# Kernel optimization log

Measured on AMD Instinct MI355X. Metric: run time of the kernel, lower is better.

## Reference

```python
import jax, jax.numpy as jnp
import numpy as np


def apply_rope(x):
    # x: [b, h, n, d], d even
    b, h, n, d = x.shape
    half = d // 2
    freqs = jnp.arange(0, half, dtype=x.dtype) / half
    theta = 1.0 / 10000 ** freqs                       # [half]
    positions = jnp.arange(n, dtype=x.dtype)
    angles = positions[:, None] * theta[None, :]       # [n, half]
    cos = jnp.cos(angles)[None, None, :, :]
    sin = jnp.sin(angles)[None, None, :, :]
    x1 = x[..., ::2]
    x2 = x[..., 1::2]
    r1 = x1 * cos - x2 * sin
    r2 = x1 * sin + x2 * cos
    # interleave r1, r2 back into even/odd lanes
    return jnp.stack([r1, r2], axis=-1).reshape(b, h, n, d)


def setup_inputs() -> dict:
    key = jax.random.key(0)
    ks = jax.random.split(key, 4)
    B, N, D = 2, 2048, 1024
    x = jax.random.normal(ks[0], (B, N, D), dtype=jnp.float32)
    w_qkv = jax.random.normal(ks[1], (D, 3 * D), dtype=jnp.float32) * (1.0 / np.sqrt(D))
    b_qkv = jnp.zeros((3 * D,), dtype=jnp.float32)
    w_out = jax.random.normal(ks[2], (D, D), dtype=jnp.float32) * (1.0 / np.sqrt(D))
    b_out = jnp.zeros((D,), dtype=jnp.float32)
    return {"x": x, "w_qkv": w_qkv, "b_qkv": b_qkv, "w_out": w_out, "b_out": b_out}


def reference(x, w_qkv, b_qkv, w_out, b_out):
    B, N, D = x.shape
    H = 16
    hd = D // H
    qkv = x @ w_qkv + b_qkv                            # [B, N, 3D]
    q, k, v = jnp.split(qkv, 3, axis=-1)
    # [B, N, D] -> [B, H, N, hd]
    to_heads = lambda t: t.reshape(B, N, H, hd).transpose(0, 2, 1, 3)
    q, k, v = to_heads(q), to_heads(k), to_heads(v)
    # ELU+1 feature map (applied BEFORE RoPE, as in source)
    q = jax.nn.elu(q) + 1
    k = jax.nn.elu(k) + 1
    rot_q = apply_rope(q)
    rot_k = apply_rope(k)
    attn_num = jnp.einsum('bhid,bhjd->bhij', rot_q, rot_k)   # [B,H,N,N]
    attn_denom = jnp.einsum('bhid,bhjd->bhij', q, k)         # [B,H,N,N]
    attn_weights = attn_num / attn_denom
    # dropout deterministic (train=False)
    out = jnp.einsum('bhij,bhjd->bhid', attn_weights, v)     # [B,H,N,hd]
    out = out.transpose(0, 2, 1, 3).reshape(B, N, D)
    return out @ w_out + b_out
```

## Files before the change

### kernel.cpp

```cpp
#include <hip/hip_runtime.h>
#include <hip/hip_bf16.h>

#define B_   2
#define N_   2048
#define D_   1024
#define H_   16
#define HD   64
#define HALF 32
#define M_   (B_*N_)
#define DQKV (3*D_)

typedef __bf16 bf16x8 __attribute__((ext_vector_type(8)));
typedef float  f32x4  __attribute__((ext_vector_type(4)));
typedef float  f32x16 __attribute__((ext_vector_type(16)));

__device__ __forceinline__ bf16x8 ldfrag(const char* tile, int row, int ch) {
    return *(const bf16x8*)(tile + row * 128 + (((ch) ^ (row & 7)) << 4));
}
__device__ __forceinline__ void stfrag16(char* tile, int row, int ch, uint4 v) {
    *(uint4*)(tile + row * 128 + (((ch) ^ (row & 7)) << 4)) = v;
}

__device__ __forceinline__ unsigned pack2(float a, float b) {
    union { __hip_bfloat16 h; unsigned short s; } x, y;
    x.h = __float2bfloat16(a); y.h = __float2bfloat16(b);
    return (unsigned)x.s | ((unsigned)y.s << 16);
}

__global__ __launch_bounds__(256) void k_tables(float* __restrict__ cos_t,
                                                float* __restrict__ sin_t) {
    int i = blockIdx.x * 256 + threadIdx.x;
    if (i >= N_ * HALF) return;
    int n = i / HALF, j = i % HALF;
    float theta = powf(10000.f, -(float)j / (float)HALF);
    float ang = (float)n * theta;
    cos_t[i] = cosf(ang);
    sin_t[i] = sinf(ang);
}

__global__ __launch_bounds__(256) void k_cvt_x(const float* __restrict__ x,
                                               __hip_bfloat16* __restrict__ xb) {
    int i = blockIdx.x * 256 + threadIdx.x;
    float4 v = ((const float4*)x)[i];
    union { ushort4 u; __hip_bfloat16 h[4]; } o;
    o.h[0] = __float2bfloat16(v.x); o.h[1] = __float2bfloat16(v.y);
    o.h[2] = __float2bfloat16(v.z); o.h[3] = __float2bfloat16(v.w);
    ((ushort4*)xb)[i] = o.u;
}

__global__ __launch_bounds__(256) void k_cvt_t(const float* __restrict__ w,
                                               __hip_bfloat16* __restrict__ wt, int ncols) {
    __shared__ float tile[32][33];
    int n0 = blockIdx.x * 32, k0 = blockIdx.y * 32;
    int tx = threadIdx.x & 31, ty = threadIdx.x >> 5;
#pragma unroll
    for (int i = 0; i < 32; i += 8)
        tile[ty + i][tx] = w[(size_t)(k0 + ty + i) * ncols + n0 + tx];
    __syncthreads();
#pragma unroll
    for (int i = 0; i < 32; i += 8)
        wt[(size_t)(n0 + ty + i) * 1024 + k0 + tx] = __float2bfloat16(tile[tx][ty + i]);
}

__global__ __launch_bounds__(256) void k_qkv(
        const __hip_bfloat16* __restrict__ xb, const __hip_bfloat16* __restrict__ wqT,
        const float* __restrict__ bias,
        const float* __restrict__ cos_t, const float* __restrict__ sin_t,
        __hip_bfloat16* __restrict__ qf, __hip_bfloat16* __restrict__ kf,
        __hip_bfloat16* __restrict__ rq, __hip_bfloat16* __restrict__ rk,
        __hip_bfloat16* __restrict__ vt) {
    __shared__ __align__(16) char sA[128 * 128];
    __shared__ __align__(16) char sB[128 * 128];

    const int t    = threadIdx.x;
    const int m0   = blockIdx.y * 128;
    const int n0w  = blockIdx.x * 128;
    const int lane = t & 63;
    const int lrow = lane & 15;
    const int lgrp = lane >> 4;
    const int wid  = t >> 6;
    const int wr   = wid >> 1;
    const int wc   = wid & 1;

    f32x4 acc[4][4] = {};

    for (int kt = 0; kt < D_ / 64; ++kt) {
        const int k0 = kt * 64;
        __syncthreads();
#pragma unroll
        for (int it = 0; it < 4; ++it) {
            int slot = it * 256 + t;
            int r = slot >> 3, c = slot & 7;
            uint4 av = *(const uint4*)(xb  + (size_t)(m0  + r) * D_ + k0 + c * 8);
            uint4 bv = *(const uint4*)(wqT + (size_t)(n0w + r) * D_ + k0 + c * 8);
            stfrag16(sA, r, c, av);
            stfrag16(sB, r, c, bv);
        }
        __syncthreads();

        bf16x8 bfr[4][2];
#pragma unroll
        for (int fn = 0; fn < 4; ++fn) {
            bfr[fn][0] = ldfrag(sB, wc * 64 + fn * 16 + lrow, lgrp);
            bfr[fn][1] = ldfrag(sB, wc * 64 + fn * 16 + lrow, 4 + lgrp);
        }
#pragma unroll
        for (int fm = 0; fm < 4; ++fm) {
            bf16x8 a0 = ldfrag(sA, wr * 64 + fm * 16 + lrow, lgrp);
            bf16x8 a1 = ldfrag(sA, wr * 64 + fm * 16 + lrow, 4 + lgrp);
#pragma unroll
            for (int fn = 0; fn < 4; ++fn) {
                acc[fm][fn] = __builtin_amdgcn_mfma_f32_16x16x32_bf16(a0, bfr[fn][0], acc[fm][fn], 0, 0, 0);
                acc[fm][fn] = __builtin_amdgcn_mfma_f32_16x16x32_bf16(a1, bfr[fn][1], acc[fm][fn], 0, 0, 0);
            }
        }
    }

#pragma unroll
    for (int fn = 0; fn < 4; ++fn) {
        int c   = n0w + wc * 64 + fn * 16 + lrow;
        int sec = c >> 10;
        int cc  = c & 1023;
        int h   = cc >> 6, dd = cc & 63;
        float bia = bias[c];
#pragma unroll
        for (int fm = 0; fm < 4; ++fm) {
            int mb = m0 + wr * 64 + fm * 16 + lgrp * 4;
            int b  = mb >> 11;
            int n  = mb & (N_ - 1);
            if (sec == 2) {
                union { ushort4 u; __hip_bfloat16 hh[4]; } pk;
#pragma unroll
                for (int r = 0; r < 4; ++r)
                    pk.hh[r] = __float2bfloat16(acc[fm][fn][r] + bia);
                *(ushort4*)(vt + ((size_t)(b * H_ + h) * HD + dd) * N_ + n) = pk.u;
            } else {
#pragma unroll
                for (int r = 0; r < 4; ++r) {
                    float val = acc[fm][fn][r] + bia;
                    float e  = val > 0.f ? val + 1.f : __expf(val);
                    float ep = __shfl_xor(e, 1);
                    int pj = dd >> 1;
                    float cs = cos_t[(n + r) * HALF + pj];
                    float sn = sin_t[(n + r) * HALF + pj];
                    float rv = (dd & 1) ? (ep * sn + e * cs) : (e * cs - ep * sn);
                    size_t o = ((size_t)(b * H_ + h) * N_ + n + r) * HD + dd;
                    if (sec == 0) { qf[o] = __float2bfloat16(e); rq[o] = __float2bfloat16(rv); }
                    else          { kf[o] = __float2bfloat16(e); rk[o] = __float2bfloat16(rv); }
                }
            }
        }
    }
}

__global__ __launch_bounds__(256, 2) void k_attn(
        const __hip_bfloat16* __restrict__ qf, const __hip_bfloat16* __restrict__ kf,
        const __hip_bfloat16* __restrict__ rq, const __hip_bfloat16* __restrict__ rk,
        const __hip_bfloat16* __restrict__ vt, __hip_bfloat16* __restrict__ ctxb) {
    __shared__ float sred[2][4096];

    const int t    = threadIdx.x;
    const int lane = t & 63;
    const int l31  = lane & 31;
    const int h    = lane >> 5;
    const int w    = t >> 6;
    const int qw   = w & 1;
    const int ks   = w >> 1;

    const int bid = blockIdx.x;
    const int swz = (bid & 7) * 64 + (bid >> 3);
    const int bh  = swz >> 4;
    const int q0  = (swz & 15) * 128;
    const size_t base = (size_t)bh * (N_ * HD);
    const int q0w = q0 + qw * 64;

    bf16x8 bq[2][4], bqe[2][4];
#pragma unroll
    for (int qb = 0; qb < 2; ++qb)
#pragma unroll
        for (int kc = 0; kc < 4; ++kc) {
            int row = q0w + qb * 32 + l31;
            int col = kc * 16 + h * 8;
            bq [qb][kc] = *(const bf16x8*)(rq + base + (size_t)row * HD + col);
            bqe[qb][kc] = *(const bf16x8*)(qf + base + (size_t)row * HD + col);
        }

    f32x16 o[2][2] = {};

    for (int r = 0; r < 16; ++r) {
        const int k0 = (2 * r + ks) * 64;
        const __hip_bfloat16* pk = rk + base + (size_t)k0 * HD + h * 8;
        const __hip_bfloat16* pe = kf + base + (size_t)k0 * HD + h * 8;

        bf16x8 wa[2][4];
#pragma unroll
        for (int kb = 0; kb < 2; ++kb) {
            bf16x8 ark[4], ake[4];
#pragma unroll
            for (int kc = 0; kc < 4; ++kc) {
                ark[kc] = *(const bf16x8*)(pk + (size_t)(kb * 32 + l31) * HD + kc * 16);
                ake[kc] = *(const bf16x8*)(pe + (size_t)(kb * 32 + l31) * HD + kc * 16);
            }
#pragma unroll
            for (int qb = 0; qb < 2; ++qb) {
                f32x16 num = {}, den = {};
#pragma unroll
                for (int kc = 0; kc < 4; ++kc)
                    num = __builtin_amdgcn_mfma_f32_32x32x16_bf16(ark[kc], bq[qb][kc], num, 0, 0, 0);
#pragma unroll
                for (int kc = 0; kc < 4; ++kc)
                    den = __builtin_amdgcn_mfma_f32_32x32x16_bf16(ake[kc], bqe[qb][kc], den, 0, 0, 0);
                unsigned u0 = pack2(num[0]  * __builtin_amdgcn_rcpf(den[0]),
                                    num[1]  * __builtin_amdgcn_rcpf(den[1]));
                unsigned u1 = pack2(num[2]  * __builtin_amdgcn_rcpf(den[2]),
                                    num[3]  * __builtin_amdgcn_rcpf(den[3]));
                unsigned u2 = pack2(num[4]  * __builtin_amdgcn_rcpf(den[4]),
                                    num[5]  * __builtin_amdgcn_rcpf(den[5]));
                unsigned u3 = pack2(num[6]  * __builtin_amdgcn_rcpf(den[6]),
                                    num[7]  * __builtin_amdgcn_rcpf(den[7]));
                unsigned u4 = pack2(num[8]  * __builtin_amdgcn_rcpf(den[8]),
                                    num[9]  * __builtin_amdgcn_rcpf(den[9]));
                unsigned u5 = pack2(num[10] * __builtin_amdgcn_rcpf(den[10]),
                                    num[11] * __builtin_amdgcn_rcpf(den[11]));
                unsigned u6 = pack2(num[12] * __builtin_amdgcn_rcpf(den[12]),
                                    num[13] * __builtin_amdgcn_rcpf(den[13]));
                unsigned u7 = pack2(num[14] * __builtin_amdgcn_rcpf(den[14]),
                                    num[15] * __builtin_amdgcn_rcpf(den[15]));
                asm volatile("v_permlane32_swap_b32 %0, %1" : "+v"(u0), "+v"(u2));
                asm volatile("v_permlane32_swap_b32 %0, %1" : "+v"(u1), "+v"(u3));
                asm volatile("v_permlane32_swap_b32 %0, %1" : "+v"(u4), "+v"(u6));
                asm volatile("v_permlane32_swap_b32 %0, %1" : "+v"(u5), "+v"(u7));
                union { unsigned uu[4]; bf16x8 v; } f0, f1;
                f0.uu[0] = u0; f0.uu[1] = u1; f0.uu[2] = u2; f0.uu[3] = u3;
                f1.uu[0] = u4; f1.uu[1] = u5; f1.uu[2] = u6; f1.uu[3] = u7;
                wa[qb][kb * 2 + 0] = f0.v;
                wa[qb][kb * 2 + 1] = f1.v;
            }
        }

#pragma unroll
        for (int db = 0; db < 2; ++db) {
            bf16x8 bv[4];
#pragma unroll
            for (int kc = 0; kc < 4; ++kc)
                bv[kc] = *(const bf16x8*)(vt + base + (size_t)(db * 32 + l31) * N_
                                          + k0 + (kc * 2 + h) * 8);
#pragma unroll
            for (int qb = 0; qb < 2; ++qb)
#pragma unroll
                for (int kc = 0; kc < 4; ++kc)
                    o[qb][db] = __builtin_amdgcn_mfma_f32_32x32x16_bf16(wa[qb][kc], bv[kc], o[qb][db], 0, 0, 0);
        }
    }

    if (ks == 1) {
#pragma unroll
        for (int qb = 0; qb < 2; ++qb)
#pragma unroll
            for (int db = 0; db < 2; ++db)
#pragma unroll
                for (int i = 0; i < 16; ++i)
                    sred[qw][(qb * 2 + db) * 1024 + i * 64 + lane] = o[qb][db][i];
    }
    __syncthreads();
    if (ks == 0) {
#pragma unroll
        for (int qb = 0; qb < 2; ++qb)
#pragma unroll
            for (int db = 0; db < 2; ++db)
#pragma unroll
                for (int i = 0; i < 16; ++i) {
                    float v = o[qb][db][i] + sred[qw][(qb * 2 + db) * 1024 + i * 64 + lane];
                    int qq = q0w + qb * 32 + (i & 3) + 8 * (i >> 2) + 4 * h;
                    ctxb[base + (size_t)qq * HD + db * 32 + l31] = __float2bfloat16(v);
                }
    }
}

__global__ __launch_bounds__(256) void k_proj(
        const __hip_bfloat16* __restrict__ ctxb, const __hip_bfloat16* __restrict__ woT,
        const float* __restrict__ bias, float* __restrict__ out) {
    __shared__ __align__(16) char sA[128 * 128];
    __shared__ __align__(16) char sB[128 * 128];

    const int t    = threadIdx.x;
    const int m0   = blockIdx.y * 128;
    const int n0w  = blockIdx.x * 128;
    const int lane = t & 63;
    const int lrow = lane & 15;
    const int lgrp = lane >> 4;
    const int wid  = t >> 6;
    const int wr   = wid >> 1;
    const int wc   = wid & 1;

    f32x4 acc[4][4] = {};

    for (int kt = 0; kt < D_ / 64; ++kt) {
        const int k0 = kt * 64;
        const int hh = k0 >> 6;
        __syncthreads();
#pragma unroll
        for (int it = 0; it < 4; ++it) {
            int slot = it * 256 + t;
            int r = slot >> 3, c = slot & 7;
            int m = m0 + r;
            int b = m >> 11, n = m & (N_ - 1);
            uint4 av = *(const uint4*)(ctxb + ((size_t)(b * H_ + hh) * N_ + n) * HD + c * 8);
            uint4 bv = *(const uint4*)(woT + (size_t)(n0w + r) * D_ + k0 + c * 8);
            stfrag16(sA, r, c, av);
            stfrag16(sB, r, c, bv);
        }
        __syncthreads();

        bf16x8 bfr[4][2];
#pragma unroll
        for (int fn = 0; fn < 4; ++fn) {
            bfr[fn][0] = ldfrag(sB, wc * 64 + fn * 16 + lrow, lgrp);
            bfr[fn][1] = ldfrag(sB, wc * 64 + fn * 16 + lrow, 4 + lgrp);
        }
#pragma unroll
        for (int fm = 0; fm < 4; ++fm) {
            bf16x8 a0 = ldfrag(sA, wr * 64 + fm * 16 + lrow, lgrp);
            bf16x8 a1 = ldfrag(sA, wr * 64 + fm * 16 + lrow, 4 + lgrp);
#pragma unroll
            for (int fn = 0; fn < 4; ++fn) {
                acc[fm][fn] = __builtin_amdgcn_mfma_f32_16x16x32_bf16(a0, bfr[fn][0], acc[fm][fn], 0, 0, 0);
                acc[fm][fn] = __builtin_amdgcn_mfma_f32_16x16x32_bf16(a1, bfr[fn][1], acc[fm][fn], 0, 0, 0);
            }
        }
    }

#pragma unroll
    for (int fn = 0; fn < 4; ++fn) {
        int c = n0w + wc * 64 + fn * 16 + lrow;
        float bia = bias[c];
#pragma unroll
        for (int fm = 0; fm < 4; ++fm) {
            int m = m0 + wr * 64 + fm * 16 + lgrp * 4;
#pragma unroll
            for (int r = 0; r < 4; ++r)
                out[(size_t)(m + r) * D_ + c] = acc[fm][fn][r] + bia;
        }
    }
}

extern "C" void kernel_launch(void* const* d_in, const int* in_sizes, int n_in,
                              void* d_out, int out_size, void* d_ws, size_t ws_size,
                              hipStream_t stream) {
    const float* x     = (const float*)d_in[0];
    const float* w_qkv = (const float*)d_in[1];
    const float* b_qkv = (const float*)d_in[2];
    const float* w_out = (const float*)d_in[3];
    const float* b_out = (const float*)d_in[4];
    float* out = (float*)d_out;

    char* ws = (char*)d_ws;
    const size_t TAB  = (size_t)N_ * HALF * sizeof(float);
    const size_t HARR = (size_t)B_ * H_ * N_ * HD * 2;
    float* cos_t = (float*)ws;
    float* sin_t = (float*)(ws + TAB);
    char* p = ws + 2 * TAB;
    __hip_bfloat16* qf  = (__hip_bfloat16*)(p);            p += HARR;
    __hip_bfloat16* kf  = (__hip_bfloat16*)(p);            p += HARR;
    __hip_bfloat16* rq  = (__hip_bfloat16*)(p);            p += HARR;
    __hip_bfloat16* rk  = (__hip_bfloat16*)(p);            p += HARR;
    __hip_bfloat16* vt  = (__hip_bfloat16*)(p);            p += HARR;
    __hip_bfloat16* xb  = (__hip_bfloat16*)(p);            p += HARR;
    __hip_bfloat16* ctxb = xb;
    __hip_bfloat16* wqT = (__hip_bfloat16*)(p);            p += (size_t)DQKV * D_ * 2;
    __hip_bfloat16* woT = (__hip_bfloat16*)(p);            p += (size_t)D_ * D_ * 2;

    hipLaunchKernelGGL(k_tables, dim3((N_ * HALF + 255) / 256), dim3(256), 0, stream,
                       cos_t, sin_t);
    hipLaunchKernelGGL(k_cvt_x, dim3(M_ * D_ / 4 / 256), dim3(256), 0, stream, x, xb);
    hipLaunchKernelGGL(k_cvt_t, dim3(DQKV / 32, D_ / 32), dim3(256), 0, stream,
                       w_qkv, wqT, DQKV);
    hipLaunchKernelGGL(k_cvt_t, dim3(D_ / 32, D_ / 32), dim3(256), 0, stream,
                       w_out, woT, D_);
    hipLaunchKernelGGL(k_qkv, dim3(DQKV / 128, M_ / 128), dim3(256), 0, stream,
                       xb, wqT, b_qkv, cos_t, sin_t, qf, kf, rq, rk, vt);
    hipLaunchKernelGGL(k_attn, dim3(512), dim3(256), 0, stream,
                       qf, kf, rq, rk, vt, ctxb);
    hipLaunchKernelGGL(k_proj, dim3(D_ / 128, M_ / 128), dim3(256), 0, stream,
                       ctxb, woT, b_out, out);
}
```

Before: 193.6 us.

## Stage K/V tiles through double-buffered LDS and widen attention blocks to 256 queries

The attention kernel now runs 512-thread blocks covering 256 queries (4 query warps x 2 key splits), so each K/V tile is shared by four query warps instead of two. K, rotated K and V^T tiles are prefetched into registers and written into a swizzled double-buffered LDS area, and MFMA fragments are read from LDS rather than directly from global memory. This cuts redundant global/L2 traffic and overlaps the next tile's loads with compute. In exchange it adds a block barrier every iteration, uses more LDS (96 KB), and halves the grid to 256 blocks, which may lower occupancy.

```diff
diff --git a/kernel.cpp b/kernel.cpp
--- a/kernel.cpp
+++ b/kernel.cpp
@@ -153,24 +153,25 @@
     }
 }
 
-__global__ __launch_bounds__(256, 2) void k_attn(
+__global__ __launch_bounds__(512, 2) void k_attn(
         const __hip_bfloat16* __restrict__ qf, const __hip_bfloat16* __restrict__ kf,
         const __hip_bfloat16* __restrict__ rq, const __hip_bfloat16* __restrict__ rk,
         const __hip_bfloat16* __restrict__ vt, __hip_bfloat16* __restrict__ ctxb) {
-    __shared__ float sred[2][4096];
+    __shared__ __align__(16) char sbuf[2][2][3 * 8192];
 
     const int t    = threadIdx.x;
     const int lane = t & 63;
     const int l31  = lane & 31;
     const int h    = lane >> 5;
-    const int w    = t >> 6;
-    const int qw   = w & 1;
-    const int ks   = w >> 1;
+    const int wid  = t >> 6;
+    const int qw   = wid & 3;
+    const int ks   = wid >> 2;
+    const int tl   = t & 255;
 
     const int bid = blockIdx.x;
-    const int swz = (bid & 7) * 64 + (bid >> 3);
-    const int bh  = swz >> 4;
-    const int q0  = (swz & 15) * 128;
+    const int swz = (bid & 7) * 32 + (bid >> 3);
+    const int bh  = swz >> 3;
+    const int q0  = (swz & 7) * 256;
     const size_t base = (size_t)bh * (N_ * HD);
     const int q0w = q0 + qw * 64;
 
@@ -185,12 +186,42 @@
             bqe[qb][kc] = *(const bf16x8*)(qf + base + (size_t)row * HD + col);
         }
 
+    uint4 st[6];
+    auto stage_load = [&](int k0) {
+#pragma unroll
+        for (int j = 0; j < 6; ++j) {
+            int slot = j * 256 + tl;
+            int ci = slot & 511, tile = slot >> 9;
+            int row = ci >> 3, cs = ci & 7;
+            int cg = cs ^ (row & 7);
+            const char* g;
+            if (tile == 0)      g = (const char*)(rk + base + (size_t)(k0 + row) * HD) + cg * 16;
+            else if (tile == 1) g = (const char*)(kf + base + (size_t)(k0 + row) * HD) + cg * 16;
+            else                g = (const char*)(vt + base + (size_t)row * N_ + k0) + cg * 16;
+            st[j] = *(const uint4*)g;
+        }
+    };
+    auto stage_write = [&](int buf) {
+#pragma unroll
+        for (int j = 0; j < 6; ++j) {
+            int slot = j * 256 + tl;
+            *(uint4*)(sbuf[ks][buf] + slot * 16) = st[j];
+        }
+    };
+
+    stage_load(ks * 64);
+    stage_write(0);
+    __syncthreads();
+
     f32x16 o[2][2] = {};
 
     for (int r = 0; r < 16; ++r) {
-        const int k0 = (2 * r + ks) * 64;
-        const __hip_bfloat16* pk = rk + base + (size_t)k0 * HD + h * 8;
-        const __hip_bfloat16* pe = kf + base + (size_t)k0 * HD + h * 8;
+        const int cur = r & 1;
+        const char* Rk = sbuf[ks][cur];
+        const char* Ke = Rk + 8192;
+        const char* Vt = Rk + 16384;
+
+        if (r + 1 < 16) stage_load((2 * (r + 1) + ks) * 64);
 
         bf16x8 wa[2][4];
 #pragma unroll
@@ -198,8 +229,8 @@
             bf16x8 ark[4], ake[4];
 #pragma unroll
             for (int kc = 0; kc < 4; ++kc) {
-                ark[kc] = *(const bf16x8*)(pk + (size_t)(kb * 32 + l31) * HD + kc * 16);
-                ake[kc] = *(const bf16x8*)(pe + (size_t)(kb * 32 + l31) * HD + kc * 16);
+                ark[kc] = ldfrag(Rk, kb * 32 + l31, kc * 2 + h);
+                ake[kc] = ldfrag(Ke, kb * 32 + l31, kc * 2 + h);
             }
 #pragma unroll
             for (int qb = 0; qb < 2; ++qb) {
@@ -243,16 +274,19 @@
             bf16x8 bv[4];
 #pragma unroll
             for (int kc = 0; kc < 4; ++kc)
-                bv[kc] = *(const bf16x8*)(vt + base + (size_t)(db * 32 + l31) * N_
-                                          + k0 + (kc * 2 + h) * 8);
+                bv[kc] = ldfrag(Vt, db * 32 + l31, kc * 2 + h);
 #pragma unroll
             for (int qb = 0; qb < 2; ++qb)
 #pragma unroll
                 for (int kc = 0; kc < 4; ++kc)
                     o[qb][db] = __builtin_amdgcn_mfma_f32_32x32x16_bf16(wa[qb][kc], bv[kc], o[qb][db], 0, 0, 0);
         }
-    }
-
+
+        if (r + 1 < 16) stage_write(cur ^ 1);
+        __syncthreads();
+    }
+
+    float* sred = (float*)sbuf;
     if (ks == 1) {
 #pragma unroll
         for (int qb = 0; qb < 2; ++qb)
@@ -260,7 +294,7 @@
             for (int db = 0; db < 2; ++db)
 #pragma unroll
                 for (int i = 0; i < 16; ++i)
-                    sred[qw][(qb * 2 + db) * 1024 + i * 64 + lane] = o[qb][db][i];
+                    sred[(((qw * 2 + qb) * 2 + db) << 10) + i * 64 + lane] = o[qb][db][i];
     }
     __syncthreads();
     if (ks == 0) {
@@ -270,7 +304,7 @@
             for (int db = 0; db < 2; ++db)
 #pragma unroll
                 for (int i = 0; i < 16; ++i) {
-                    float v = o[qb][db][i] + sred[qw][(qb * 2 + db) * 1024 + i * 64 + lane];
+                    float v = o[qb][db][i] + sred[(((qw * 2 + qb) * 2 + db) << 10) + i * 64 + lane];
                     int qq = q0w + qb * 32 + (i & 3) + 8 * (i >> 2) + 4 * h;
                     ctxb[base + (size_t)qq * HD + db * 32 + l31] = __float2bfloat16(v);
                 }
@@ -379,7 +413,7 @@
                        w_out, woT, D_);
     hipLaunchKernelGGL(k_qkv, dim3(DQKV / 128, M_ / 128), dim3(256), 0, stream,
                        xb, wqT, b_qkv, cos_t, sin_t, qf, kf, rq, rk, vt);
-    hipLaunchKernelGGL(k_attn, dim3(512), dim3(256), 0, stream,
+    hipLaunchKernelGGL(k_attn, dim3(256), dim3(512), 0, stream,
                        qf, kf, rq, rk, vt, ctxb);
     hipLaunchKernelGGL(k_proj, dim3(D_ / 128, M_ / 128), dim3(256), 0, stream,
                        ctxb, woT, b_out, out);
```

After: 181.5 us. -6.3%, faster.
